# Kernel optimization log

Hardware: AMD Instinct MI355X
Metric: run time of the kernel (lower is better)

## Reference

```python
import jax, jax.numpy as jnp
import numpy as np

EMA_DECAY = 0.99
EPS = 1e-5
KSZ = 4096
D = 512

def setup_inputs() -> dict:
    key = jax.random.key(0)
    k1, k2 = jax.random.split(key)
    f_ipm = jax.random.normal(k1, (8, 4096, D), dtype=jnp.float32)
    K = jax.random.normal(k2, (KSZ, D), dtype=jnp.float32)
    ema_cluster_size = jnp.zeros((KSZ,), dtype=jnp.float32)
    ema_w = K  # buffer initialized as K.clone() in the torch module
    return {"f_ipm": f_ipm, "K": K, "ema_cluster_size": ema_cluster_size, "ema_w": ema_w}

def _cdist_sq(x, y):
    # squared euclidean pairwise distances [N, M]; argmin over these equals
    # argmin over torch.cdist (sqrt is monotonic)
    x2 = jnp.sum(x * x, axis=-1, keepdims=True)
    y2 = jnp.sum(y * y, axis=-1)
    return jnp.maximum(x2 + y2[None, :] - 2.0 * (x @ y.T), 0.0)

def reference(f_ipm, K, ema_cluster_size, ema_w):
    # Training-mode forward of IPLM with EMA codebook update (functional).
    B, T, d = f_ipm.shape
    Ksz = K.shape[0]
    f = f_ipm.reshape(-1, d)                     # [N, D]
    d2 = _cdist_sq(f, K)                         # [N, Ksz]
    k1_idx = jnp.argmin(d2, axis=1)              # [N]
    k1 = K[k1_idx]                               # [N, D] gather
    loss_lk = jnp.mean((jax.lax.stop_gradient(k1) - f) ** 2)
    # EMA cluster statistics via segment_sum (equivalent to one_hot.T @ f)
    counts = jax.ops.segment_sum(jnp.ones((f.shape[0],), f.dtype), k1_idx, num_segments=Ksz)
    dw = jax.ops.segment_sum(f, k1_idx, num_segments=Ksz)
    new_ecs = ema_cluster_size * EMA_DECAY + (1.0 - EMA_DECAY) * counts
    n = new_ecs.sum()
    smoothed = (new_ecs + EPS) / (n + Ksz * EPS) * n
    new_ema_w = ema_w * EMA_DECAY + (1.0 - EMA_DECAY) * dw
    new_K = new_ema_w / smoothed[:, None]
    f_ipmlm = k1.reshape(B, T, d)
    return (f_ipmlm, loss_lk, new_K, new_ecs, new_ema_w)
```

## Files before the change

### kernel.cpp

```cpp
#include <hip/hip_runtime.h>
#include <hip/hip_bf16.h>

#define NROWS 32768
#define DDIM  512
#define KSZ_  4096
#define EMA_DECAY_ 0.99f
#define EPS_ 1e-5f

#define BM 128
#define BN 128
#define NCHUNK 4
#define CSPLIT 8
#define BKB 64

typedef float f32x4 __attribute__((ext_vector_type(4)));
typedef __bf16 bf16x8 __attribute__((ext_vector_type(8)));

__device__ __forceinline__ void g2lds16(const __bf16* g, __bf16* l) {
    __builtin_amdgcn_global_load_lds(
        (const __attribute__((address_space(1))) void*)g,
        (__attribute__((address_space(3))) void*)l, 16, 0, 0);
}

__device__ __forceinline__ void cvt8(const float4 x0, const float4 x1,
                                     bf16x8& h, bf16x8& l) {
    float xs[8] = {x0.x, x0.y, x0.z, x0.w, x1.x, x1.y, x1.z, x1.w};
#pragma unroll
    for (int j = 0; j < 8; j++) {
        __bf16 hj = (__bf16)xs[j];
        h[j] = hj;
        l[j] = (__bf16)(xs[j] - (float)hj);
    }
}

__global__ __launch_bounds__(256) void convert_kernel(
    const float* __restrict__ src,
    __bf16* __restrict__ hi, __bf16* __restrict__ lo) {
    int g  = blockIdx.x * 256 + threadIdx.x;
    int s  = g & 7;
    int r  = (g >> 3) & 127;
    int ks = (g >> 10) & 7;
    int rb = g >> 13;
    int srck = ks * 64 + ((s ^ (r & 7)) * 8);
    const float* p = src + (size_t)(rb * 128 + r) * DDIM + srck;
    float4 x0 = *(const float4*)p;
    float4 x1 = *(const float4*)(p + 4);
    bf16x8 h, l;
    cvt8(x0, x1, h, l);
    *(bf16x8*)(hi + (size_t)g * 8) = h;
    *(bf16x8*)(lo + (size_t)g * 8) = l;
}

__global__ __launch_bounds__(256) void kt2_kernel(const float* __restrict__ K,
                                                  float* __restrict__ Kt2) {
    int gid  = blockIdx.x * 256 + threadIdx.x;
    int row  = gid >> 6;
    int lane = threadIdx.x & 63;
    const float* kr = K + (size_t)row * DDIM;
    float s = 0.f;
#pragma unroll
    for (int u = 0; u < 2; u++) {
        float4 v = *(const float4*)&kr[u * 256 + lane * 4];
        s += v.x * v.x + v.y * v.y + v.z * v.z + v.w * v.w;
    }
#pragma unroll
    for (int off = 1; off < 64; off <<= 1) s += __shfl_xor(s, off, 64);
    if (lane == 0) Kt2[row] = s;
}

__global__ __launch_bounds__(256, 2) void argmin_kernel(
    const __bf16* __restrict__ fh, const __bf16* __restrict__ fl,
    const __bf16* __restrict__ kh, const __bf16* __restrict__ kl,
    const float* __restrict__ Kt2,
    float* __restrict__ bestd, int* __restrict__ bestidx) {

    __shared__ __align__(16) __bf16 Ah[BM * BKB];
    __shared__ __align__(16) __bf16 Al[BM * BKB];
    __shared__ __align__(16) __bf16 Bh[BN * BKB];
    __shared__ __align__(16) __bf16 Bl[BN * BKB];
    __shared__ float redD[2][BM];
    __shared__ int   redI[2][BM];

    const int tid  = threadIdx.x;
    const int lane = tid & 63;
    const int w    = tid >> 6;
    const int wr   = w >> 1;
    const int wc   = w & 1;
    const int l15  = lane & 15;
    const int l4   = lane >> 4;
    const int rb   = blockIdx.x;
    const int split = blockIdx.y;

    float best[16];
    int   bidx[16];
#pragma unroll
    for (int i = 0; i < 16; i++) { best[i] = 3.4e38f; bidx[i] = 0x7fffffff; }

    for (int chunk = 0; chunk < NCHUNK; ++chunk) {
        const int cb = split * NCHUNK + chunk;
        const int c0 = cb * BN;
        f32x4 acc[4][4];
#pragma unroll
        for (int m = 0; m < 4; m++)
#pragma unroll
            for (int n = 0; n < 4; n++)
                acc[m][n] = (f32x4){0.f, 0.f, 0.f, 0.f};

        for (int ks = 0; ks < DDIM / BKB; ++ks) {
            const __bf16* tAh = fh + (size_t)(rb * 8 + ks) * (BM * BKB);
            const __bf16* tAl = fl + (size_t)(rb * 8 + ks) * (BM * BKB);
            const __bf16* tBh = kh + (size_t)(cb * 8 + ks) * (BN * BKB);
            const __bf16* tBl = kl + (size_t)(cb * 8 + ks) * (BN * BKB);
            __syncthreads();
#pragma unroll
            for (int i = 0; i < 4; i++) {
                const int gg  = i * 256 + tid;
                const int ub  = (i * 256 + w * 64) * 8;
                g2lds16(tAh + (size_t)gg * 8, Ah + ub);
                g2lds16(tAl + (size_t)gg * 8, Al + ub);
                g2lds16(tBh + (size_t)gg * 8, Bh + ub);
                g2lds16(tBl + (size_t)gg * 8, Bl + ub);
            }
            __syncthreads();

#pragma unroll
            for (int h = 0; h < 2; ++h) {
                bf16x8 av[4], alv[4], bv[4], blv[4];
#pragma unroll
                for (int m = 0; m < 4; m++) {
                    int row  = wr * 64 + m * 16 + l15;
                    int slot = (h * 4 + l4) ^ (l15 & 7);
                    int off  = row * BKB + slot * 8;
                    av[m]  = *(const bf16x8*)&Ah[off];
                    alv[m] = *(const bf16x8*)&Al[off];
                }
#pragma unroll
                for (int n = 0; n < 4; n++) {
                    int row  = wc * 64 + n * 16 + l15;
                    int slot = (h * 4 + l4) ^ (l15 & 7);
                    int off  = row * BKB + slot * 8;
                    bv[n]  = *(const bf16x8*)&Bh[off];
                    blv[n] = *(const bf16x8*)&Bl[off];
                }
#pragma unroll
                for (int m = 0; m < 4; m++)
#pragma unroll
                    for (int n = 0; n < 4; n++)
                        acc[m][n] = __builtin_amdgcn_mfma_f32_16x16x32_bf16(av[m], bv[n], acc[m][n], 0, 0, 0);
#pragma unroll
                for (int m = 0; m < 4; m++)
#pragma unroll
                    for (int n = 0; n < 4; n++)
                        acc[m][n] = __builtin_amdgcn_mfma_f32_16x16x32_bf16(av[m], blv[n], acc[m][n], 0, 0, 0);
#pragma unroll
                for (int m = 0; m < 4; m++)
#pragma unroll
                    for (int n = 0; n < 4; n++)
                        acc[m][n] = __builtin_amdgcn_mfma_f32_16x16x32_bf16(alv[m], bv[n], acc[m][n], 0, 0, 0);
            }
        }

        float kt2c[4];
#pragma unroll
        for (int n = 0; n < 4; n++) kt2c[n] = Kt2[c0 + wc * 64 + n * 16 + l15];
#pragma unroll
        for (int m = 0; m < 4; m++)
#pragma unroll
            for (int q = 0; q < 4; q++) {
                float d = 3.4e38f; int bi = 0x7fffffff;
#pragma unroll
                for (int n = 0; n < 4; n++) {
                    float s = 0.5f * kt2c[n] - acc[m][n][q];
                    int col = c0 + wc * 64 + n * 16 + l15;
                    if (s < d || (s == d && col < bi)) { d = s; bi = col; }
                }
                int i16 = m * 4 + q;
                if (d < best[i16] || (d == best[i16] && bi < bidx[i16])) {
                    best[i16] = d; bidx[i16] = bi;
                }
            }
    }

#pragma unroll
    for (int i = 0; i < 16; i++) {
        float d = best[i]; int bi = bidx[i];
#pragma unroll
        for (int off = 1; off < 16; off <<= 1) {
            float od = __shfl_xor(d, off, 64);
            int   oi = __shfl_xor(bi, off, 64);
            if (od < d || (od == d && oi < bi)) { d = od; bi = oi; }
        }
        if (l15 == 0) {
            int m = i >> 2, q = i & 3;
            int rl = wr * 64 + m * 16 + l4 * 4 + q;
            redD[wc][rl] = d;
            redI[wc][rl] = bi;
        }
    }
    __syncthreads();
    if (tid < BM) {
        float d0 = redD[0][tid], d1 = redD[1][tid];
        int   i0 = redI[0][tid], i1 = redI[1][tid];
        if (d1 < d0 || (d1 == d0 && i1 < i0)) { d0 = d1; i0 = i1; }
        bestd[(size_t)(rb * BM + tid) * CSPLIT + split]   = d0;
        bestidx[(size_t)(rb * BM + tid) * CSPLIT + split] = i0;
    }
}

__global__ __launch_bounds__(256) void reduce_kernel(
    const float* __restrict__ bestd, const int* __restrict__ bestidx,
    int* __restrict__ k1, int* __restrict__ cnt) {
    int row = blockIdx.x * 256 + threadIdx.x;
    float4 d0 = *(const float4*)&bestd[(size_t)row * CSPLIT];
    float4 d1 = *(const float4*)&bestd[(size_t)row * CSPLIT + 4];
    int4   i0 = *(const int4*)&bestidx[(size_t)row * CSPLIT];
    int4   i1 = *(const int4*)&bestidx[(size_t)row * CSPLIT + 4];
    float ds[8] = {d0.x, d0.y, d0.z, d0.w, d1.x, d1.y, d1.z, d1.w};
    int   is[8] = {i0.x, i0.y, i0.z, i0.w, i1.x, i1.y, i1.z, i1.w};
    float d = ds[0]; int bi = is[0];
#pragma unroll
    for (int s = 1; s < 8; s++)
        if (ds[s] < d || (ds[s] == d && is[s] < bi)) { d = ds[s]; bi = is[s]; }
    k1[row] = bi;
    atomicAdd(&cnt[bi], 1);
}

__global__ __launch_bounds__(256) void scan_kernel(
    const int* __restrict__ cnt, int* __restrict__ offs) {
    __shared__ int sums[256];
    int t = threadIdx.x;
    int local[16];
    int s = 0;
#pragma unroll
    for (int i = 0; i < 16; i++) { local[i] = cnt[t * 16 + i]; s += local[i]; }
    sums[t] = s;
    __syncthreads();
    for (int off = 1; off < 256; off <<= 1) {
        int v = (t >= off) ? sums[t - off] : 0;
        __syncthreads();
        sums[t] += v;
        __syncthreads();
    }
    int run = sums[t] - s;
#pragma unroll
    for (int i = 0; i < 16; i++) { offs[t * 16 + i] = run; run += local[i]; }
}

__global__ __launch_bounds__(256) void scatter_kernel(
    const int* __restrict__ k1, const int* __restrict__ offs,
    int* __restrict__ cursor, int* __restrict__ bucket) {
    int row = blockIdx.x * 256 + threadIdx.x;
    int bi = k1[row];
    int pos = atomicAdd(&cursor[bi], 1);
    bucket[offs[bi] + pos] = row;
}

__global__ __launch_bounds__(256) void gather_kernel(
    const float* __restrict__ f, const float* __restrict__ K,
    const int* __restrict__ k1,
    float* __restrict__ out_fipm, float* __restrict__ loss_sum) {
    __shared__ float ls[4];
    int tid  = threadIdx.x;
    int wid  = (blockIdx.x * 256 + tid) >> 6;
    int lane = tid & 63;
    float lsum = 0.f;
#pragma unroll
    for (int rr = 0; rr < 8; rr++) {
        int row = wid * 8 + rr;
        int bi  = k1[row];
        const float* frow = f + (size_t)row * DDIM;
        const float* krow = K + (size_t)bi * DDIM;
#pragma unroll
        for (int u = 0; u < 2; u++) {
            int off = u * 256 + lane * 4;
            float4 fv = *(const float4*)&frow[off];
            float4 kv = *(const float4*)&krow[off];
            *(float4*)&out_fipm[(size_t)row * DDIM + off] = kv;
            float dx = kv.x - fv.x, dy = kv.y - fv.y;
            float dz = kv.z - fv.z, dwv = kv.w - fv.w;
            lsum += dx * dx + dy * dy + dz * dz + dwv * dwv;
        }
    }
#pragma unroll
    for (int off = 1; off < 64; off <<= 1) lsum += __shfl_xor(lsum, off, 64);
    if (lane == 0) ls[tid >> 6] = lsum;
    __syncthreads();
    if (tid == 0) atomicAdd(loss_sum, ls[0] + ls[1] + ls[2] + ls[3]);
}

__global__ __launch_bounds__(256) void dw_kernel(
    const float* __restrict__ f, const int* __restrict__ offs,
    const int* __restrict__ cnt, const int* __restrict__ bucket,
    float* __restrict__ dw) {
    int j = blockIdx.x;
    int t = threadIdx.x;
    int beg = offs[j];
    int c   = cnt[j];
    float2 acc = {0.f, 0.f};
    int i = 0;
    for (; i + 1 < c; i += 2) {
        int r0 = bucket[beg + i];
        int r1 = bucket[beg + i + 1];
        float2 a = *(const float2*)&f[(size_t)r0 * DDIM + t * 2];
        float2 b = *(const float2*)&f[(size_t)r1 * DDIM + t * 2];
        acc.x += a.x + b.x;
        acc.y += a.y + b.y;
    }
    if (i < c) {
        int r0 = bucket[beg + i];
        float2 a = *(const float2*)&f[(size_t)r0 * DDIM + t * 2];
        acc.x += a.x;
        acc.y += a.y;
    }
    *(float2*)&dw[(size_t)j * DDIM + t * 2] = acc;
}

__global__ __launch_bounds__(256) void ecs_kernel(
    const float* __restrict__ ecs_in, const int* __restrict__ cnt,
    float* __restrict__ out_ecs, float* __restrict__ n_sum) {
    int i = blockIdx.x * 256 + threadIdx.x;
    float v = ecs_in[i] * EMA_DECAY_ + (1.0f - EMA_DECAY_) * (float)cnt[i];
    out_ecs[i] = v;
    float s = v;
#pragma unroll
    for (int off = 1; off < 64; off <<= 1) s += __shfl_xor(s, off, 64);
    if ((threadIdx.x & 63) == 0) atomicAdd(n_sum, s);
}

__global__ __launch_bounds__(256) void final_kernel(
    const float* __restrict__ ema_w, const float* __restrict__ dw,
    const float* __restrict__ out_ecs, const float* __restrict__ n_sum,
    const float* __restrict__ loss_sum,
    float* __restrict__ out_K, float* __restrict__ out_emaw,
    float* __restrict__ out_loss) {
    int idx4 = blockIdx.x * 256 + threadIdx.x;
    int row  = idx4 >> 7;
    float n  = *n_sum;
    float smoothed = (out_ecs[row] + EPS_) / (n + KSZ_ * EPS_) * n;
    float inv = 1.0f / smoothed;
    size_t e = (size_t)idx4 * 4;
    float4 wv = *(const float4*)&ema_w[e];
    float4 dv = *(const float4*)&dw[e];
    float w0 = EMA_DECAY_ * wv.x + (1.0f - EMA_DECAY_) * dv.x;
    float w1 = EMA_DECAY_ * wv.y + (1.0f - EMA_DECAY_) * dv.y;
    float w2 = EMA_DECAY_ * wv.z + (1.0f - EMA_DECAY_) * dv.z;
    float w3 = EMA_DECAY_ * wv.w + (1.0f - EMA_DECAY_) * dv.w;
    out_emaw[e + 0] = w0; out_emaw[e + 1] = w1;
    out_emaw[e + 2] = w2; out_emaw[e + 3] = w3;
    out_K[e + 0] = w0 * inv; out_K[e + 1] = w1 * inv;
    out_K[e + 2] = w2 * inv; out_K[e + 3] = w3 * inv;
    if (idx4 == 0) *out_loss = *loss_sum * (1.0f / 16777216.0f);
}

extern "C" void kernel_launch(void* const* d_in, const int* in_sizes, int n_in,
                              void* d_out, int out_size, void* d_ws, size_t ws_size,
                              hipStream_t stream) {
    const float* f     = (const float*)d_in[0];
    const float* K     = (const float*)d_in[1];
    const float* ecs   = (const float*)d_in[2];
    const float* ema_w = (const float*)d_in[3];

    float* ws       = (float*)d_ws;
    float* Kt2      = ws;
    float* bestd    = ws + 4096;
    int*   bestidx  = (int*)(ws + 266240);
    float* dw       = ws + 528384;
    float* loss_sum = ws + 2625536;
    float* n_sum    = ws + 2625537;
    int*   cnt      = (int*)(ws + 2625538);
    int*   cursor   = (int*)(ws + 2629634);
    int*   offs     = (int*)(ws + 2633730);
    int*   k1       = (int*)(ws + 2637826);
    int*   bucket   = (int*)(ws + 2670594);
    __bf16* fh      = (__bf16*)(ws + 2703364);
    __bf16* fl      = (__bf16*)(ws + 11091972);
    __bf16* kh      = (__bf16*)(ws + 19480580);
    __bf16* kl      = (__bf16*)(ws + 20529156);

    float* out      = (float*)d_out;
    float* out_fipm = out;
    float* out_loss = out + 16777216;
    float* out_K    = out + 16777217;
    float* out_ecs  = out + 18874369;
    float* out_emaw = out + 18878465;

    hipMemsetAsync(loss_sum, 0, (size_t)(2 + 4096 + 4096) * sizeof(float), stream);

    convert_kernel<<<NROWS * DDIM / 8 / 256, 256, 0, stream>>>(f, fh, fl);
    convert_kernel<<<KSZ_ * DDIM / 8 / 256, 256, 0, stream>>>(K, kh, kl);

    kt2_kernel<<<KSZ_ * 64 / 256, 256, 0, stream>>>(K, Kt2);

    dim3 grid(NROWS / BM, CSPLIT);
    argmin_kernel<<<grid, 256, 0, stream>>>(fh, fl, kh, kl, Kt2, bestd, bestidx);

    reduce_kernel<<<NROWS / 256, 256, 0, stream>>>(bestd, bestidx, k1, cnt);
    scan_kernel<<<1, 256, 0, stream>>>(cnt, offs);
    scatter_kernel<<<NROWS / 256, 256, 0, stream>>>(k1, offs, cursor, bucket);

    gather_kernel<<<NROWS / 8 / 4, 256, 0, stream>>>(f, K, k1, out_fipm, loss_sum);

    dw_kernel<<<KSZ_, 256, 0, stream>>>(f, offs, cnt, bucket, dw);

    ecs_kernel<<<KSZ_ / 256, 256, 0, stream>>>(ecs, cnt, out_ecs, n_sum);

    final_kernel<<<(KSZ_ * DDIM / 4) / 256, 256, 0, stream>>>(
        ema_w, dw, out_ecs, n_sum, loss_sum, out_K, out_emaw, out_loss);
}
```

Baseline: 695.2 us.

## Enlarge argmin GEMM tiles, double-buffer LDS, fuse dw with final EMA update

The argmin GEMM moves from 128x128 tiles with 4 waves to 256x256 tiles with 8 waves (512 threads). The three split-bf16 passes are flattened into a single 24-step K loop, and loads for the next step are double-buffered in LDS while the current step computes. Raising MFMA priority and doing per-tile column reduction inside the loop cut synchronisation and global traffic per FLOP. The dw and final kernels are fused so the dw intermediate is never written to memory. In exchange, register and LDS pressure rise and the grid gets coarser, which may hurt occupancy and wave balance.

```diff
diff --git a/kernel.cpp b/kernel.cpp
--- a/kernel.cpp
+++ b/kernel.cpp
@@ -7,11 +7,11 @@
 #define EMA_DECAY_ 0.99f
 #define EPS_ 1e-5f
 
-#define BM 128
-#define BN 128
-#define NCHUNK 4
-#define CSPLIT 8
+#define BMW 256
+#define BNW 256
+#define CSPLIT 16
 #define BKB 64
+#define NKS 24
 
 typedef float f32x4 __attribute__((ext_vector_type(4)));
 typedef __bf16 bf16x8 __attribute__((ext_vector_type(8)));
@@ -68,142 +68,131 @@
     if (lane == 0) Kt2[row] = s;
 }
 
-__global__ __launch_bounds__(256, 2) void argmin_kernel(
+__global__ __launch_bounds__(512, 2) void argmin_kernel(
     const __bf16* __restrict__ fh, const __bf16* __restrict__ fl,
     const __bf16* __restrict__ kh, const __bf16* __restrict__ kl,
     const float* __restrict__ Kt2,
     float* __restrict__ bestd, int* __restrict__ bestidx) {
 
-    __shared__ __align__(16) __bf16 Ah[BM * BKB];
-    __shared__ __align__(16) __bf16 Al[BM * BKB];
-    __shared__ __align__(16) __bf16 Bh[BN * BKB];
-    __shared__ __align__(16) __bf16 Bl[BN * BKB];
-    __shared__ float redD[2][BM];
-    __shared__ int   redI[2][BM];
+    __shared__ __align__(16) __bf16 Abuf[2][BMW * BKB];
+    __shared__ __align__(16) __bf16 Bbuf[2][BNW * BKB];
+    __shared__ float redD[4][BMW];
+    __shared__ int   redI[4][BMW];
 
     const int tid  = threadIdx.x;
     const int lane = tid & 63;
     const int w    = tid >> 6;
-    const int wr   = w >> 1;
-    const int wc   = w & 1;
+    const int wr   = w >> 2;
+    const int wc   = w & 3;
     const int l15  = lane & 15;
     const int l4   = lane >> 4;
-    const int rb   = blockIdx.x;
-    const int split = blockIdx.y;
-
-    float best[16];
-    int   bidx[16];
-#pragma unroll
-    for (int i = 0; i < 16; i++) { best[i] = 3.4e38f; bidx[i] = 0x7fffffff; }
-
-    for (int chunk = 0; chunk < NCHUNK; ++chunk) {
-        const int cb = split * NCHUNK + chunk;
-        const int c0 = cb * BN;
-        f32x4 acc[4][4];
-#pragma unroll
-        for (int m = 0; m < 4; m++)
-#pragma unroll
-            for (int n = 0; n < 4; n++)
-                acc[m][n] = (f32x4){0.f, 0.f, 0.f, 0.f};
-
-        for (int ks = 0; ks < DDIM / BKB; ++ks) {
-            const __bf16* tAh = fh + (size_t)(rb * 8 + ks) * (BM * BKB);
-            const __bf16* tAl = fl + (size_t)(rb * 8 + ks) * (BM * BKB);
-            const __bf16* tBh = kh + (size_t)(cb * 8 + ks) * (BN * BKB);
-            const __bf16* tBl = kl + (size_t)(cb * 8 + ks) * (BN * BKB);
-            __syncthreads();
-#pragma unroll
-            for (int i = 0; i < 4; i++) {
-                const int gg  = i * 256 + tid;
-                const int ub  = (i * 256 + w * 64) * 8;
-                g2lds16(tAh + (size_t)gg * 8, Ah + ub);
-                g2lds16(tAl + (size_t)gg * 8, Al + ub);
-                g2lds16(tBh + (size_t)gg * 8, Bh + ub);
-                g2lds16(tBl + (size_t)gg * 8, Bl + ub);
-            }
-            __syncthreads();
-
-#pragma unroll
-            for (int h = 0; h < 2; ++h) {
-                bf16x8 av[4], alv[4], bv[4], blv[4];
-#pragma unroll
-                for (int m = 0; m < 4; m++) {
-                    int row  = wr * 64 + m * 16 + l15;
-                    int slot = (h * 4 + l4) ^ (l15 & 7);
-                    int off  = row * BKB + slot * 8;
-                    av[m]  = *(const bf16x8*)&Ah[off];
-                    alv[m] = *(const bf16x8*)&Al[off];
-                }
-#pragma unroll
-                for (int n = 0; n < 4; n++) {
-                    int row  = wc * 64 + n * 16 + l15;
-                    int slot = (h * 4 + l4) ^ (l15 & 7);
-                    int off  = row * BKB + slot * 8;
-                    bv[n]  = *(const bf16x8*)&Bh[off];
-                    blv[n] = *(const bf16x8*)&Bl[off];
-                }
-#pragma unroll
-                for (int m = 0; m < 4; m++)
-#pragma unroll
-                    for (int n = 0; n < 4; n++)
-                        acc[m][n] = __builtin_amdgcn_mfma_f32_16x16x32_bf16(av[m], bv[n], acc[m][n], 0, 0, 0);
-#pragma unroll
-                for (int m = 0; m < 4; m++)
-#pragma unroll
-                    for (int n = 0; n < 4; n++)
-                        acc[m][n] = __builtin_amdgcn_mfma_f32_16x16x32_bf16(av[m], blv[n], acc[m][n], 0, 0, 0);
-#pragma unroll
-                for (int m = 0; m < 4; m++)
-#pragma unroll
-                    for (int n = 0; n < 4; n++)
-                        acc[m][n] = __builtin_amdgcn_mfma_f32_16x16x32_bf16(alv[m], bv[n], acc[m][n], 0, 0, 0);
-            }
-        }
-
-        float kt2c[4];
-#pragma unroll
-        for (int n = 0; n < 4; n++) kt2c[n] = Kt2[c0 + wc * 64 + n * 16 + l15];
-#pragma unroll
-        for (int m = 0; m < 4; m++)
-#pragma unroll
-            for (int q = 0; q < 4; q++) {
-                float d = 3.4e38f; int bi = 0x7fffffff;
-#pragma unroll
-                for (int n = 0; n < 4; n++) {
-                    float s = 0.5f * kt2c[n] - acc[m][n][q];
-                    int col = c0 + wc * 64 + n * 16 + l15;
-                    if (s < d || (s == d && col < bi)) { d = s; bi = col; }
-                }
-                int i16 = m * 4 + q;
-                if (d < best[i16] || (d == best[i16] && bi < bidx[i16])) {
-                    best[i16] = d; bidx[i16] = bi;
-                }
-            }
-    }
-
-#pragma unroll
-    for (int i = 0; i < 16; i++) {
-        float d = best[i]; int bi = bidx[i];
-#pragma unroll
-        for (int off = 1; off < 16; off <<= 1) {
-            float od = __shfl_xor(d, off, 64);
-            int   oi = __shfl_xor(bi, off, 64);
+    const int bx   = blockIdx.x;
+    const int by   = blockIdx.y;
+
+    f32x4 acc[8][4];
+#pragma unroll
+    for (int m = 0; m < 8; m++)
+#pragma unroll
+        for (int n = 0; n < 4; n++)
+            acc[m][n] = (f32x4){0.f, 0.f, 0.f, 0.f};
+
+    auto STAGE = [&](int t, int b) {
+        const __bf16* aArr = (t < 16) ? fh : fl;
+        const __bf16* bArr = (t < 8) ? kh : ((t < 16) ? kl : kh);
+        const int pks = t & 7;
+#pragma unroll
+        for (int i = 0; i < 4; i++) {
+            int g   = i * 512 + tid;
+            int sub = g >> 10;
+            int gg  = g & 1023;
+            const __bf16* src =
+                aArr + ((size_t)(((bx * 2 + sub) * 8 + pks) * 1024 + gg)) * 8;
+            g2lds16(src, &Abuf[b][(i * 512 + w * 64) * 8]);
+        }
+#pragma unroll
+        for (int i = 0; i < 4; i++) {
+            int g   = i * 512 + tid;
+            int sub = g >> 10;
+            int gg  = g & 1023;
+            const __bf16* src =
+                bArr + ((size_t)(((by * 2 + sub) * 8 + pks) * 1024 + gg)) * 8;
+            g2lds16(src, &Bbuf[b][(i * 512 + w * 64) * 8]);
+        }
+    };
+
+    STAGE(0, 0);
+    __syncthreads();
+
+    int cur = 0;
+    for (int t = 0; t < NKS; ++t) {
+        if (t + 1 < NKS) STAGE(t + 1, cur ^ 1);
+#pragma unroll
+        for (int khf = 0; khf < 2; ++khf) {
+            bf16x8 av[8], bv[4];
+#pragma unroll
+            for (int m = 0; m < 8; m++) {
+                int r = wr * 128 + m * 16 + l15;
+                int s = (khf * 4 + l4) ^ (l15 & 7);
+                int gran = ((r >> 7) << 10) + ((r & 127) << 3) + s;
+                av[m] = *(const bf16x8*)&Abuf[cur][gran * 8];
+            }
+#pragma unroll
+            for (int n = 0; n < 4; n++) {
+                int r = wc * 64 + n * 16 + l15;
+                int s = (khf * 4 + l4) ^ (l15 & 7);
+                int gran = ((r >> 7) << 10) + ((r & 127) << 3) + s;
+                bv[n] = *(const bf16x8*)&Bbuf[cur][gran * 8];
+            }
+            __builtin_amdgcn_s_setprio(1);
+#pragma unroll
+            for (int m = 0; m < 8; m++)
+#pragma unroll
+                for (int n = 0; n < 4; n++)
+                    acc[m][n] = __builtin_amdgcn_mfma_f32_16x16x32_bf16(
+                        av[m], bv[n], acc[m][n], 0, 0, 0);
+            __builtin_amdgcn_s_setprio(0);
+        }
+        __syncthreads();
+        cur ^= 1;
+    }
+
+    const int c0 = by * 256;
+    float kt2c[4];
+#pragma unroll
+    for (int n = 0; n < 4; n++) kt2c[n] = Kt2[c0 + wc * 64 + n * 16 + l15];
+#pragma unroll
+    for (int m = 0; m < 8; m++)
+#pragma unroll
+        for (int q = 0; q < 4; q++) {
+            float d = 3.4e38f; int bi = 0x7fffffff;
+#pragma unroll
+            for (int n = 0; n < 4; n++) {
+                float sc = 0.5f * kt2c[n] - acc[m][n][q];
+                int col = c0 + wc * 64 + n * 16 + l15;
+                if (sc < d || (sc == d && col < bi)) { d = sc; bi = col; }
+            }
+#pragma unroll
+            for (int off = 1; off < 16; off <<= 1) {
+                float od = __shfl_xor(d, off, 64);
+                int   oi = __shfl_xor(bi, off, 64);
+                if (od < d || (od == d && oi < bi)) { d = od; bi = oi; }
+            }
+            if (l15 == 0) {
+                int rl = wr * 128 + m * 16 + l4 * 4 + q;
+                redD[wc][rl] = d;
+                redI[wc][rl] = bi;
+            }
+        }
+    __syncthreads();
+    if (tid < BMW) {
+        float d = redD[0][tid]; int bi = redI[0][tid];
+#pragma unroll
+        for (int c = 1; c < 4; c++) {
+            float od = redD[c][tid]; int oi = redI[c][tid];
             if (od < d || (od == d && oi < bi)) { d = od; bi = oi; }
         }
-        if (l15 == 0) {
-            int m = i >> 2, q = i & 3;
-            int rl = wr * 64 + m * 16 + l4 * 4 + q;
-            redD[wc][rl] = d;
-            redI[wc][rl] = bi;
-        }
-    }
-    __syncthreads();
-    if (tid < BM) {
-        float d0 = redD[0][tid], d1 = redD[1][tid];
-        int   i0 = redI[0][tid], i1 = redI[1][tid];
-        if (d1 < d0 || (d1 == d0 && i1 < i0)) { d0 = d1; i0 = i1; }
-        bestd[(size_t)(rb * BM + tid) * CSPLIT + split]   = d0;
-        bestidx[(size_t)(rb * BM + tid) * CSPLIT + split] = i0;
+        bestd[(size_t)(bx * BMW + tid) * CSPLIT + by]   = d;
+        bestidx[(size_t)(bx * BMW + tid) * CSPLIT + by] = bi;
     }
 }
 
@@ -211,16 +200,17 @@
     const float* __restrict__ bestd, const int* __restrict__ bestidx,
     int* __restrict__ k1, int* __restrict__ cnt) {
     int row = blockIdx.x * 256 + threadIdx.x;
-    float4 d0 = *(const float4*)&bestd[(size_t)row * CSPLIT];
-    float4 d1 = *(const float4*)&bestd[(size_t)row * CSPLIT + 4];
-    int4   i0 = *(const int4*)&bestidx[(size_t)row * CSPLIT];
-    int4   i1 = *(const int4*)&bestidx[(size_t)row * CSPLIT + 4];
-    float ds[8] = {d0.x, d0.y, d0.z, d0.w, d1.x, d1.y, d1.z, d1.w};
-    int   is[8] = {i0.x, i0.y, i0.z, i0.w, i1.x, i1.y, i1.z, i1.w};
-    float d = ds[0]; int bi = is[0];
-#pragma unroll
-    for (int s = 1; s < 8; s++)
-        if (ds[s] < d || (ds[s] == d && is[s] < bi)) { d = ds[s]; bi = is[s]; }
+    float d = 3.4e38f; int bi = 0x7fffffff;
+#pragma unroll
+    for (int v = 0; v < 4; v++) {
+        float4 dv = *(const float4*)&bestd[(size_t)row * CSPLIT + v * 4];
+        int4   iv = *(const int4*)&bestidx[(size_t)row * CSPLIT + v * 4];
+        float ds[4] = {dv.x, dv.y, dv.z, dv.w};
+        int   is[4] = {iv.x, iv.y, iv.z, iv.w};
+#pragma unroll
+        for (int s = 0; s < 4; s++)
+            if (ds[s] < d || (ds[s] == d && is[s] < bi)) { d = ds[s]; bi = is[s]; }
+    }
     k1[row] = bi;
     atomicAdd(&cnt[bi], 1);
 }
@@ -288,10 +278,26 @@
     if (tid == 0) atomicAdd(loss_sum, ls[0] + ls[1] + ls[2] + ls[3]);
 }
 
-__global__ __launch_bounds__(256) void dw_kernel(
-    const float* __restrict__ f, const int* __restrict__ offs,
-    const int* __restrict__ cnt, const int* __restrict__ bucket,
-    float* __restrict__ dw) {
+__global__ __launch_bounds__(256) void ecs_kernel(
+    const float* __restrict__ ecs_in, const int* __restrict__ cnt,
+    float* __restrict__ out_ecs, float* __restrict__ n_sum) {
+    int i = blockIdx.x * 256 + threadIdx.x;
+    float v = ecs_in[i] * EMA_DECAY_ + (1.0f - EMA_DECAY_) * (float)cnt[i];
+    out_ecs[i] = v;
+    float s = v;
+#pragma unroll
+    for (int off = 1; off < 64; off <<= 1) s += __shfl_xor(s, off, 64);
+    if ((threadIdx.x & 63) == 0) atomicAdd(n_sum, s);
+}
+
+__global__ __launch_bounds__(256) void dwfinal_kernel(
+    const float* __restrict__ f, const float* __restrict__ ema_w,
+    const int* __restrict__ offs, const int* __restrict__ cnt,
+    const int* __restrict__ bucket,
+    const float* __restrict__ out_ecs, const float* __restrict__ n_sum,
+    const float* __restrict__ loss_sum,
+    float* __restrict__ out_K, float* __restrict__ out_emaw,
+    float* __restrict__ out_loss) {
     int j = blockIdx.x;
     int t = threadIdx.x;
     int beg = offs[j];
@@ -312,44 +318,16 @@
         acc.x += a.x;
         acc.y += a.y;
     }
-    *(float2*)&dw[(size_t)j * DDIM + t * 2] = acc;
-}
-
-__global__ __launch_bounds__(256) void ecs_kernel(
-    const float* __restrict__ ecs_in, const int* __restrict__ cnt,
-    float* __restrict__ out_ecs, float* __restrict__ n_sum) {
-    int i = blockIdx.x * 256 + threadIdx.x;
-    float v = ecs_in[i] * EMA_DECAY_ + (1.0f - EMA_DECAY_) * (float)cnt[i];
-    out_ecs[i] = v;
-    float s = v;
-#pragma unroll
-    for (int off = 1; off < 64; off <<= 1) s += __shfl_xor(s, off, 64);
-    if ((threadIdx.x & 63) == 0) atomicAdd(n_sum, s);
-}
-
-__global__ __launch_bounds__(256) void final_kernel(
-    const float* __restrict__ ema_w, const float* __restrict__ dw,
-    const float* __restrict__ out_ecs, const float* __restrict__ n_sum,
-    const float* __restrict__ loss_sum,
-    float* __restrict__ out_K, float* __restrict__ out_emaw,
-    float* __restrict__ out_loss) {
-    int idx4 = blockIdx.x * 256 + threadIdx.x;
-    int row  = idx4 >> 7;
-    float n  = *n_sum;
-    float smoothed = (out_ecs[row] + EPS_) / (n + KSZ_ * EPS_) * n;
+    float n = *n_sum;
+    float smoothed = (out_ecs[j] + EPS_) / (n + KSZ_ * EPS_) * n;
     float inv = 1.0f / smoothed;
-    size_t e = (size_t)idx4 * 4;
-    float4 wv = *(const float4*)&ema_w[e];
-    float4 dv = *(const float4*)&dw[e];
-    float w0 = EMA_DECAY_ * wv.x + (1.0f - EMA_DECAY_) * dv.x;
-    float w1 = EMA_DECAY_ * wv.y + (1.0f - EMA_DECAY_) * dv.y;
-    float w2 = EMA_DECAY_ * wv.z + (1.0f - EMA_DECAY_) * dv.z;
-    float w3 = EMA_DECAY_ * wv.w + (1.0f - EMA_DECAY_) * dv.w;
+    float2 wv = *(const float2*)&ema_w[(size_t)j * DDIM + t * 2];
+    float w0 = EMA_DECAY_ * wv.x + (1.0f - EMA_DECAY_) * acc.x;
+    float w1 = EMA_DECAY_ * wv.y + (1.0f - EMA_DECAY_) * acc.y;
+    size_t e = (size_t)j * DDIM + t * 2;
     out_emaw[e + 0] = w0; out_emaw[e + 1] = w1;
-    out_emaw[e + 2] = w2; out_emaw[e + 3] = w3;
     out_K[e + 0] = w0 * inv; out_K[e + 1] = w1 * inv;
-    out_K[e + 2] = w2 * inv; out_K[e + 3] = w3 * inv;
-    if (idx4 == 0) *out_loss = *loss_sum * (1.0f / 16777216.0f);
+    if (j == 0 && t == 0) *out_loss = *loss_sum * (1.0f / 16777216.0f);
 }
 
 extern "C" void kernel_launch(void* const* d_in, const int* in_sizes, int n_in,
@@ -363,19 +341,18 @@
     float* ws       = (float*)d_ws;
     float* Kt2      = ws;
     float* bestd    = ws + 4096;
-    int*   bestidx  = (int*)(ws + 266240);
-    float* dw       = ws + 528384;
-    float* loss_sum = ws + 2625536;
-    float* n_sum    = ws + 2625537;
-    int*   cnt      = (int*)(ws + 2625538);
-    int*   cursor   = (int*)(ws + 2629634);
-    int*   offs     = (int*)(ws + 2633730);
-    int*   k1       = (int*)(ws + 2637826);
-    int*   bucket   = (int*)(ws + 2670594);
-    __bf16* fh      = (__bf16*)(ws + 2703364);
-    __bf16* fl      = (__bf16*)(ws + 11091972);
-    __bf16* kh      = (__bf16*)(ws + 19480580);
-    __bf16* kl      = (__bf16*)(ws + 20529156);
+    int*   bestidx  = (int*)(ws + 528384);
+    float* loss_sum = ws + 1052672;
+    float* n_sum    = ws + 1052673;
+    int*   cnt      = (int*)(ws + 1052674);
+    int*   cursor   = (int*)(ws + 1056770);
+    int*   offs     = (int*)(ws + 1060866);
+    int*   k1       = (int*)(ws + 1064962);
+    int*   bucket   = (int*)(ws + 1097730);
+    __bf16* fh      = (__bf16*)(ws + 1130498);
+    __bf16* fl      = (__bf16*)(ws + 9519106);
+    __bf16* kh      = (__bf16*)(ws + 17907714);
+    __bf16* kl      = (__bf16*)(ws + 18956290);
 
     float* out      = (float*)d_out;
     float* out_fipm = out;
@@ -391,19 +368,18 @@
 
     kt2_kernel<<<KSZ_ * 64 / 256, 256, 0, stream>>>(K, Kt2);
 
-    dim3 grid(NROWS / BM, CSPLIT);
-    argmin_kernel<<<grid, 256, 0, stream>>>(fh, fl, kh, kl, Kt2, bestd, bestidx);
+    dim3 grid(NROWS / BMW, CSPLIT);
+    argmin_kernel<<<grid, 512, 0, stream>>>(fh, fl, kh, kl, Kt2, bestd, bestidx);
 
     reduce_kernel<<<NROWS / 256, 256, 0, stream>>>(bestd, bestidx, k1, cnt);
     scan_kernel<<<1, 256, 0, stream>>>(cnt, offs);
     scatter_kernel<<<NROWS / 256, 256, 0, stream>>>(k1, offs, cursor, bucket);
 
+    ecs_kernel<<<KSZ_ / 256, 256, 0, stream>>>(ecs, cnt, out_ecs, n_sum);
+
     gather_kernel<<<NROWS / 8 / 4, 256, 0, stream>>>(f, K, k1, out_fipm, loss_sum);
 
-    dw_kernel<<<KSZ_, 256, 0, stream>>>(f, offs, cnt, bucket, dw);
-
-    ecs_kernel<<<KSZ_ / 256, 256, 0, stream>>>(ecs, cnt, out_ecs, n_sum);
-
-    final_kernel<<<(KSZ_ * DDIM / 4) / 256, 256, 0, stream>>>(
-        ema_w, dw, out_ecs, n_sum, loss_sum, out_K, out_emaw, out_loss);
-}
+    dwfinal_kernel<<<KSZ_, 256, 0, stream>>>(
+        f, ema_w, offs, cnt, bucket, out_ecs, n_sum, loss_sum,
+        out_K, out_emaw, out_loss);
+}
```

Result: slower. 968.2 us (+39.3%).
